# Kernel tuning notes

Hardware: AMD Instinct MI355X
Metric: run time of the kernel (lower is better)

## Reference

```python
import jax, jax.numpy as jnp
import numpy as np

DECAY = 0.99
EPS = 1e-05


def setup_inputs() -> dict:
    key = jax.random.key(0)
    k1, k2 = jax.random.split(key)
    x = jax.random.normal(k1, (32, 2048, 128), dtype=jnp.float32)
    embed = jax.random.normal(k2, (1024, 128), dtype=jnp.float32)
    cluster_size = jnp.zeros((1024,), dtype=jnp.float32)
    embed_avg = embed  # register_buffer('embed_avg', embed.clone())
    return {"x": x, "embed": embed, "cluster_size": cluster_size, "embed_avg": embed_avg}


def reference(x, embed, cluster_size, embed_avg):
    N, D = embed.shape
    flat_x = x.reshape(-1, D)  # [T, D]
    distances = (
        jnp.sum(flat_x * flat_x, axis=1, keepdims=True)
        + jnp.sum(embed * embed, axis=1)
        - 2.0 * flat_x @ embed.T
    )  # [T, N]
    idx = jnp.argmin(distances, axis=1)  # [T]
    quantized = embed[idx].reshape(x.shape)
    # EMA codebook update (training branch); segment_sum replaces the one-hot matmuls
    counts = jax.ops.segment_sum(jnp.ones(flat_x.shape[0], dtype=x.dtype), idx, num_segments=N)
    embed_sums = jax.ops.segment_sum(flat_x, idx, num_segments=N)  # [N, D]
    new_cluster_size = DECAY * cluster_size + (1.0 - DECAY) * counts
    new_embed_avg = DECAY * embed_avg + (1.0 - DECAY) * embed_sums
    n = jnp.sum(new_cluster_size)
    cs = (new_cluster_size + EPS) / (n + N * EPS) * n
    new_embed = new_embed_avg / cs[:, None]
    # straight-through estimator
    out = x + jax.lax.stop_gradient(quantized - x)
    return out, new_embed, new_cluster_size, new_embed_avg
```

## Files before the change

### kernel.cpp

```cpp
#include <hip/hip_runtime.h>

#define NTOK   65536
#define NCODES 1024
#define DIM    128
#define BT     128
#define MARGIN 6.0f
#define CAP    2047

typedef __attribute__((ext_vector_type(8))) short short8;
typedef __attribute__((ext_vector_type(4))) float f32x4;
typedef const __attribute__((address_space(1))) char gchar_t;
typedef __attribute__((address_space(3))) char lchar_t;

__device__ __forceinline__ unsigned short f2bf(float f) {
  unsigned u = __float_as_uint(f);
  u += 0x7FFFu + ((u >> 16) & 1u);
  return (unsigned short)(u >> 16);
}

__global__ __launch_bounds__(256) void ee_kernel(const float* __restrict__ E,
                                                 float* __restrict__ ee) {
  #pragma clang fp contract(off)
  int c = blockIdx.x * blockDim.x + threadIdx.x;
  if (c >= NCODES) return;
  const float4* r4 = (const float4*)(E + (size_t)c * DIM);
  float v[DIM];
  #pragma unroll
  for (int i = 0; i < 32; ++i) {
    float4 q = r4[i];
    v[4*i] = q.x; v[4*i+1] = q.y; v[4*i+2] = q.z; v[4*i+3] = q.w;
  }
  float r[8];
  #pragma unroll
  for (int j = 0; j < 8; ++j) r[j] = v[j] * v[j];
  #pragma unroll
  for (int i = 1; i < 16; ++i) {
    #pragma unroll
    for (int j = 0; j < 8; ++j) { float s = v[8*i+j] * v[8*i+j]; r[j] = r[j] + s; }
  }
  ee[c] = ((r[0]+r[1])+(r[2]+r[3])) + ((r[4]+r[5])+(r[6]+r[7]));
}

__global__ __launch_bounds__(256) void ebf_kernel(const float* __restrict__ E,
                                                  unsigned short* __restrict__ ebf) {
  const int id = blockIdx.x * 256 + threadIdx.x;
  const int l  = id & 63;
  const int s  = (id >> 6) & 3;
  const int ct = id >> 8;
  const int c  = ct * 16 + (l & 15);
  const int ko = s * 32 + (l >> 4) * 8;
  const float4* p = (const float4*)(E + (size_t)c * DIM + ko);
  float4 A = p[0], B = p[1];
  short8 v;
  v[0]=f2bf(A.x); v[1]=f2bf(A.y); v[2]=f2bf(A.z); v[3]=f2bf(A.w);
  v[4]=f2bf(B.x); v[5]=f2bf(B.y); v[6]=f2bf(B.z); v[7]=f2bf(B.w);
  ((short8*)ebf)[id] = v;
}

__global__ __launch_bounds__(256, 2) void vq_main(
    const float* __restrict__ X, const float* __restrict__ E,
    const unsigned short* __restrict__ ebf, const float* __restrict__ ee,
    float* __restrict__ out, int* __restrict__ idxg, int* __restrict__ cnt_i) {
  #pragma clang fp contract(off)
  __shared__ __align__(16) char e_lds[2 * 32768];
  __shared__ __align__(16) char region[10240];

  const int tid  = threadIdx.x;
  const int lane = tid & 63;
  const int wv   = tid >> 6;
  const long blk = blockIdx.x;
  const float* Xb = X + (size_t)blk * BT * DIM;

  float* thrf = (float*)region;
  unsigned long long* best64 = (unsigned long long*)(region + 512);
  int*      cand_n = (int*)(region + 1536);
  unsigned* cand   = (unsigned*)(region + 1540);

#define STAGE_E(CT, BUF)                                                      \
  {                                                                           \
    _Pragma("unroll")                                                         \
    for (int q = 0; q < 8; ++q) {                                             \
      const int u = wv * 8 + q;                                               \
      gchar_t* src = (gchar_t*)((const char*)ebf                              \
                      + ((size_t)(((CT) * 32 + u) * 64 + lane) << 4));        \
      lchar_t* dst = (lchar_t*)(e_lds + (BUF) * 32768 + u * 1024);            \
      __builtin_amdgcn_global_load_lds(                                       \
          (const __attribute__((address_space(1))) void*)src,                 \
          (__attribute__((address_space(3))) void*)dst, 16, 0, 0);            \
    }                                                                         \
  }

  STAGE_E(0, 0)

  short8 afr[2][4];
  #pragma unroll
  for (int t2 = 0; t2 < 2; ++t2) {
    const int row = (wv * 2 + t2) * 16 + (lane & 15);
    #pragma unroll
    for (int s = 0; s < 4; ++s) {
      const float4* p = (const float4*)(Xb + row * DIM + (s * 4 + (lane >> 4)) * 8);
      float4 A = p[0], B = p[1];
      short8 v;
      v[0]=f2bf(A.x); v[1]=f2bf(A.y); v[2]=f2bf(A.z); v[3]=f2bf(A.w);
      v[4]=f2bf(B.x); v[5]=f2bf(B.y); v[6]=f2bf(B.z); v[7]=f2bf(B.w);
      afr[t2][s] = v;
    }
  }

  float bv[2][4];
  #pragma unroll
  for (int t2 = 0; t2 < 2; ++t2)
    #pragma unroll
    for (int rg = 0; rg < 4; ++rg) bv[t2][rg] = __builtin_inff();

  asm volatile("s_waitcnt vmcnt(0)" ::: "memory");
  __syncthreads();

  for (int ctile = 0; ctile < 8; ++ctile) {
    if (ctile < 7) STAGE_E(ctile + 1, (ctile + 1) & 1)
    const char* eb = e_lds + (ctile & 1) * 32768;
    #pragma unroll 2
    for (int ct = 0; ct < 8; ++ct) {
      short8 b0 = *(const short8*)(eb + (ct * 4 + 0) * 1024 + lane * 16);
      short8 b1 = *(const short8*)(eb + (ct * 4 + 1) * 1024 + lane * 16);
      short8 b2 = *(const short8*)(eb + (ct * 4 + 2) * 1024 + lane * 16);
      short8 b3 = *(const short8*)(eb + (ct * 4 + 3) * 1024 + lane * 16);
      float eevv = ee[ctile * 128 + ct * 16 + (lane & 15)];
      #pragma unroll
      for (int t2 = 0; t2 < 2; ++t2) {
        f32x4 acc = {0.f, 0.f, 0.f, 0.f};
        acc = __builtin_amdgcn_mfma_f32_16x16x32_bf16(afr[t2][0], b0, acc, 0, 0, 0);
        acc = __builtin_amdgcn_mfma_f32_16x16x32_bf16(afr[t2][1], b1, acc, 0, 0, 0);
        acc = __builtin_amdgcn_mfma_f32_16x16x32_bf16(afr[t2][2], b2, acc, 0, 0, 0);
        acc = __builtin_amdgcn_mfma_f32_16x16x32_bf16(afr[t2][3], b3, acc, 0, 0, 0);
        #pragma unroll
        for (int rg = 0; rg < 4; ++rg) {
          float d = eevv - 2.0f * acc[rg];
          if (d < bv[t2][rg]) bv[t2][rg] = d;
        }
      }
    }
    asm volatile("s_waitcnt vmcnt(0)" ::: "memory");
    __syncthreads();
  }

  #pragma unroll
  for (int t2 = 0; t2 < 2; ++t2)
    #pragma unroll
    for (int rg = 0; rg < 4; ++rg) {
      float b = bv[t2][rg];
      #pragma unroll
      for (int m = 1; m < 16; m <<= 1) {
        float pb = __shfl_xor(b, m, 64);
        if (pb < b) b = pb;
      }
      if ((lane & 15) == 0)
        thrf[(wv * 2 + t2) * 16 + (lane >> 4) * 4 + rg] = b + MARGIN;
    }
  __syncthreads();
  if (tid < 128) best64[tid] = ~0ull;
  if (tid == 0) *cand_n = 0;
  __syncthreads();

  float thv[2][4];
  #pragma unroll
  for (int t2 = 0; t2 < 2; ++t2)
    #pragma unroll
    for (int rg = 0; rg < 4; ++rg)
      thv[t2][rg] = thrf[(wv * 2 + t2) * 16 + (lane >> 4) * 4 + rg];

  STAGE_E(0, 0)
  asm volatile("s_waitcnt vmcnt(0)" ::: "memory");
  __syncthreads();
  for (int ctile = 0; ctile < 8; ++ctile) {
    if (ctile < 7) STAGE_E(ctile + 1, (ctile + 1) & 1)
    const char* eb = e_lds + (ctile & 1) * 32768;
    #pragma unroll 2
    for (int ct = 0; ct < 8; ++ct) {
      short8 b0 = *(const short8*)(eb + (ct * 4 + 0) * 1024 + lane * 16);
      short8 b1 = *(const short8*)(eb + (ct * 4 + 1) * 1024 + lane * 16);
      short8 b2 = *(const short8*)(eb + (ct * 4 + 2) * 1024 + lane * 16);
      short8 b3 = *(const short8*)(eb + (ct * 4 + 3) * 1024 + lane * 16);
      float eevv = ee[ctile * 128 + ct * 16 + (lane & 15)];
      const int code = ctile * 128 + ct * 16 + (lane & 15);
      #pragma unroll
      for (int t2 = 0; t2 < 2; ++t2) {
        f32x4 acc = {0.f, 0.f, 0.f, 0.f};
        acc = __builtin_amdgcn_mfma_f32_16x16x32_bf16(afr[t2][0], b0, acc, 0, 0, 0);
        acc = __builtin_amdgcn_mfma_f32_16x16x32_bf16(afr[t2][1], b1, acc, 0, 0, 0);
        acc = __builtin_amdgcn_mfma_f32_16x16x32_bf16(afr[t2][2], b2, acc, 0, 0, 0);
        acc = __builtin_amdgcn_mfma_f32_16x16x32_bf16(afr[t2][3], b3, acc, 0, 0, 0);
        #pragma unroll
        for (int rg = 0; rg < 4; ++rg) {
          float d = eevv - 2.0f * acc[rg];
          if (d < thv[t2][rg]) {
            int slot = atomicAdd(cand_n, 1);
            if (slot < CAP) {
              const int token = (wv * 2 + t2) * 16 + (lane >> 4) * 4 + rg;
              cand[slot] = ((unsigned)token << 10) | (unsigned)code;
            }
          }
        }
      }
    }
    asm volatile("s_waitcnt vmcnt(0)" ::: "memory");
    __syncthreads();
  }
  __syncthreads();

  {
    int cn = *cand_n;
    const int nc = cn < CAP ? cn : CAP;
    for (int i = tid; i < nc; i += 256) {
      const unsigned pc = cand[i];
      const int t = pc >> 10, c = pc & 1023;
      const float* xr = Xb + t * DIM;
      const float* er = E + (size_t)c * DIM;
      float dot = 0.0f;
      #pragma unroll
      for (int k = 0; k < DIM; ++k) dot = __builtin_fmaf(xr[k], er[k], dot);
      float d = ee[c] - 2.0f * dot;
      unsigned u = __float_as_uint(d);
      u ^= (unsigned)((int)u >> 31) | 0x80000000u;
      unsigned long long key = ((unsigned long long)u << 32) | (unsigned)c;
      atomicMin(best64 + t, key);
    }
  }
  __syncthreads();

  if (tid < BT) {
    const int c0 = (int)(best64[tid] & 1023ull);
    idxg[blk * BT + tid] = c0;
    atomicAdd(cnt_i + c0, 1);
  }
  const int tt2 = tid >> 1, hf = tid & 1;
  const int fi2 = (int)(best64[tt2] & 1023ull);
  const float* xrow = Xb  + tt2 * DIM + hf * 64;
  const float* erow = E   + ((size_t)fi2 << 7) + hf * 64;
  float*       orow = out + ((size_t)blk * BT + tt2) * DIM + hf * 64;
  #pragma unroll
  for (int q = 0; q < 16; ++q) {
    float4 xv = *(const float4*)(xrow + q * 4);
    float4 ev = *(const float4*)(erow + q * 4);
    float4 o;
    o.x = xv.x + (ev.x - xv.x);
    o.y = xv.y + (ev.y - xv.y);
    o.z = xv.z + (ev.z - xv.z);
    o.w = xv.w + (ev.w - xv.w);
    *(float4*)(orow + q * 4) = o;
  }
}

__global__ __launch_bounds__(1024) void prefix_fin1(
    const float* __restrict__ cluster_size, const int* __restrict__ cnt_i,
    float* __restrict__ out_cs, float* __restrict__ cs_ws,
    int* __restrict__ cursor, int* __restrict__ offs) {
  #pragma clang fp contract(off)
  __shared__ float red[1024];
  __shared__ int   sc[1024];
  const int n = threadIdx.x;
  const int cnt = cnt_i[n];
  float ncs = 0.99f * cluster_size[n] + 0.01f * (float)cnt;
  out_cs[n] = ncs;
  red[n] = ncs;
  sc[n]  = cnt;
  __syncthreads();
  for (int s = 512; s > 0; s >>= 1) {
    if (n < s) red[n] = red[n] + red[n + s];
    __syncthreads();
  }
  float ntot = red[0];
  cs_ws[n] = (ncs + 1e-5f) / (ntot + 0.01024f) * ntot;
  for (int d = 1; d < 1024; d <<= 1) {
    int t = (n >= d) ? sc[n - d] : 0;
    __syncthreads();
    sc[n] += t;
    __syncthreads();
  }
  int excl = sc[n] - cnt;
  cursor[n] = excl;
  offs[n]   = excl;
}

__global__ __launch_bounds__(256) void scatter_kernel(
    const int* __restrict__ idxg, int* __restrict__ cursor,
    int* __restrict__ order) {
  const int t  = blockIdx.x * 256 + threadIdx.x;
  const int fi = idxg[t];
  const int slot = atomicAdd(cursor + fi, 1);
  order[slot] = t;
}

__global__ __launch_bounds__(256) void sums_chunk(
    const float* __restrict__ X, const int* __restrict__ order,
    const int* __restrict__ idxg, float* __restrict__ sums) {
  #pragma clang fp contract(off)
  const int lane = threadIdx.x & 63;
  const int base = blockIdx.x * 256 + (threadIdx.x >> 6) * 64;
  const int tl = order[base + lane];
  const int cl = idxg[tl];
  float ax = 0.f, ay = 0.f;
  int cprev = __shfl(cl, 0, 64);
  #pragma unroll
  for (int j0 = 0; j0 < 64; j0 += 8) {
    int tj[8], cj[8];
    float2 buf[8];
    #pragma unroll
    for (int q = 0; q < 8; ++q) tj[q] = __shfl(tl, j0 + q, 64);
    #pragma unroll
    for (int q = 0; q < 8; ++q)
      buf[q] = *((const float2*)(X + ((size_t)tj[q] << 7)) + lane);
    #pragma unroll
    for (int q = 0; q < 8; ++q) cj[q] = __shfl(cl, j0 + q, 64);
    #pragma unroll
    for (int q = 0; q < 8; ++q) {
      if (cj[q] != cprev) {
        atomicAdd(sums + cprev * DIM + lane * 2,     ax);
        atomicAdd(sums + cprev * DIM + lane * 2 + 1, ay);
        ax = 0.f; ay = 0.f; cprev = cj[q];
      }
      ax = ax + buf[q].x;
      ay = ay + buf[q].y;
    }
  }
  atomicAdd(sums + cprev * DIM + lane * 2,     ax);
  atomicAdd(sums + cprev * DIM + lane * 2 + 1, ay);
}

__global__ __launch_bounds__(256) void finalize2(
    const float* __restrict__ embed_avg, const float* __restrict__ sums,
    const float* __restrict__ cs_ws, float* __restrict__ out_embed,
    float* __restrict__ out_avg) {
  #pragma clang fp contract(off)
  int i = blockIdx.x * 256 + threadIdx.x;
  float av = 0.99f * embed_avg[i] + 0.01f * sums[i];
  out_avg[i]   = av;
  out_embed[i] = av / cs_ws[i >> 7];
}

extern "C" void kernel_launch(void* const* d_in, const int* in_sizes, int n_in,
                              void* d_out, int out_size, void* d_ws, size_t ws_size,
                              hipStream_t stream) {
  const float* X  = (const float*)d_in[0];
  const float* E  = (const float*)d_in[1];
  const float* CS = (const float*)d_in[2];
  const float* EA = (const float*)d_in[3];
  float* out = (float*)d_out;
  float* ws  = (float*)d_ws;

  int*   cnt_i  = (int*)ws;
  float* sums   = ws + 1024;
  float* eearr  = ws + 132096;
  float* csarr  = ws + 133120;
  int*   cursor = (int*)(ws + 134144);
  int*   offs   = (int*)(ws + 135168);
  int*   idxarr = (int*)(ws + 136192);
  int*   order  = (int*)(ws + 201728);
  unsigned short* ebf = (unsigned short*)(ws + 267264);

  hipMemsetAsync(d_ws, 0, 132096 * sizeof(float), stream);

  ee_kernel     <<<NCODES / 256, 256, 0, stream>>>(E, eearr);
  ebf_kernel    <<<64,           256, 0, stream>>>(E, ebf);
  vq_main       <<<NTOK / BT,    256, 0, stream>>>(X, E, ebf, eearr, out,
                                                   idxarr, cnt_i);
  prefix_fin1   <<<1, 1024, 0, stream>>>(CS, cnt_i, out + 8519680, csarr,
                                         cursor, offs);
  scatter_kernel<<<NTOK / 256,   256, 0, stream>>>(idxarr, cursor, order);
  sums_chunk    <<<NTOK / 256,   256, 0, stream>>>(X, order, idxarr, sums);
  finalize2     <<<131072 / 256, 256, 0, stream>>>(EA, sums, csarr,
                                                   out + 8388608, out + 8520704);
}
```

Measured before the change: 173.0 us.

## Keep codebook slices in registers and stream X tiles from LDS; merge prep kernels

Reverses the main loop's data reuse. Each wave now holds a 512-code slice of the bf16 codebook in registers, and the block's 128 tokens are staged once in LDS in MFMA fragment layout. This replaces the double-buffered global-to-LDS codebook staging and its per-tile barriers. Per-wave partial minima go to shared memory and are combined into the per-token thresholds. The two codebook preprocessing kernels are merged into one launch. The cost is a large register footprint (32 short8 fragments per wave), which may hurt occupancy under launch_bounds(256,2) or cause spills.

```diff
diff --git a/kernel.cpp b/kernel.cpp
--- a/kernel.cpp
+++ b/kernel.cpp
@@ -9,8 +9,6 @@
 
 typedef __attribute__((ext_vector_type(8))) short short8;
 typedef __attribute__((ext_vector_type(4))) float f32x4;
-typedef const __attribute__((address_space(1))) char gchar_t;
-typedef __attribute__((address_space(3))) char lchar_t;
 
 __device__ __forceinline__ unsigned short f2bf(float f) {
   unsigned u = __float_as_uint(f);
@@ -18,43 +16,43 @@
   return (unsigned short)(u >> 16);
 }
 
-__global__ __launch_bounds__(256) void ee_kernel(const float* __restrict__ E,
-                                                 float* __restrict__ ee) {
-  #pragma clang fp contract(off)
-  int c = blockIdx.x * blockDim.x + threadIdx.x;
-  if (c >= NCODES) return;
-  const float4* r4 = (const float4*)(E + (size_t)c * DIM);
-  float v[DIM];
-  #pragma unroll
-  for (int i = 0; i < 32; ++i) {
-    float4 q = r4[i];
-    v[4*i] = q.x; v[4*i+1] = q.y; v[4*i+2] = q.z; v[4*i+3] = q.w;
-  }
-  float r[8];
-  #pragma unroll
-  for (int j = 0; j < 8; ++j) r[j] = v[j] * v[j];
-  #pragma unroll
-  for (int i = 1; i < 16; ++i) {
-    #pragma unroll
-    for (int j = 0; j < 8; ++j) { float s = v[8*i+j] * v[8*i+j]; r[j] = r[j] + s; }
-  }
-  ee[c] = ((r[0]+r[1])+(r[2]+r[3])) + ((r[4]+r[5])+(r[6]+r[7]));
-}
-
-__global__ __launch_bounds__(256) void ebf_kernel(const float* __restrict__ E,
-                                                  unsigned short* __restrict__ ebf) {
-  const int id = blockIdx.x * 256 + threadIdx.x;
-  const int l  = id & 63;
-  const int s  = (id >> 6) & 3;
-  const int ct = id >> 8;
-  const int c  = ct * 16 + (l & 15);
-  const int ko = s * 32 + (l >> 4) * 8;
-  const float4* p = (const float4*)(E + (size_t)c * DIM + ko);
-  float4 A = p[0], B = p[1];
-  short8 v;
-  v[0]=f2bf(A.x); v[1]=f2bf(A.y); v[2]=f2bf(A.z); v[3]=f2bf(A.w);
-  v[4]=f2bf(B.x); v[5]=f2bf(B.y); v[6]=f2bf(B.z); v[7]=f2bf(B.w);
-  ((short8*)ebf)[id] = v;
+__global__ __launch_bounds__(256) void prep_kernel(const float* __restrict__ E,
+                                                   float* __restrict__ ee,
+                                                   unsigned short* __restrict__ ebf) {
+  #pragma clang fp contract(off)
+  const int b = blockIdx.x;
+  if (b < 64) {
+    const int id = b * 256 + threadIdx.x;
+    const int l  = id & 63;
+    const int s  = (id >> 6) & 3;
+    const int ct = id >> 8;
+    const int c  = ct * 16 + (l & 15);
+    const int ko = s * 32 + (l >> 4) * 8;
+    const float4* p = (const float4*)(E + (size_t)c * DIM + ko);
+    float4 A = p[0], B = p[1];
+    short8 v;
+    v[0]=f2bf(A.x); v[1]=f2bf(A.y); v[2]=f2bf(A.z); v[3]=f2bf(A.w);
+    v[4]=f2bf(B.x); v[5]=f2bf(B.y); v[6]=f2bf(B.z); v[7]=f2bf(B.w);
+    ((short8*)ebf)[id] = v;
+  } else {
+    const int c = (b - 64) * 256 + threadIdx.x;
+    const float4* r4 = (const float4*)(E + (size_t)c * DIM);
+    float v[DIM];
+    #pragma unroll
+    for (int i = 0; i < 32; ++i) {
+      float4 q = r4[i];
+      v[4*i] = q.x; v[4*i+1] = q.y; v[4*i+2] = q.z; v[4*i+3] = q.w;
+    }
+    float r[8];
+    #pragma unroll
+    for (int j = 0; j < 8; ++j) r[j] = v[j] * v[j];
+    #pragma unroll
+    for (int i = 1; i < 16; ++i) {
+      #pragma unroll
+      for (int j = 0; j < 8; ++j) { float s = v[8*i+j] * v[8*i+j]; r[j] = r[j] + s; }
+    }
+    ee[c] = ((r[0]+r[1])+(r[2]+r[3])) + ((r[4]+r[5])+(r[6]+r[7]));
+  }
 }
 
 __global__ __launch_bounds__(256, 2) void vq_main(
@@ -62,8 +60,12 @@
     const unsigned short* __restrict__ ebf, const float* __restrict__ ee,
     float* __restrict__ out, int* __restrict__ idxg, int* __restrict__ cnt_i) {
   #pragma clang fp contract(off)
-  __shared__ __align__(16) char e_lds[2 * 32768];
-  __shared__ __align__(16) char region[10240];
+  __shared__ __align__(16) char x_lds[32768];
+  __shared__ float bestA[4][BT];
+  __shared__ float thrf[BT];
+  __shared__ unsigned long long best64[BT];
+  __shared__ int cand_n;
+  __shared__ unsigned cand[CAP];
 
   const int tid  = threadIdx.x;
   const int lane = tid & 63;
@@ -71,145 +73,133 @@
   const long blk = blockIdx.x;
   const float* Xb = X + (size_t)blk * BT * DIM;
 
-  float* thrf = (float*)region;
-  unsigned long long* best64 = (unsigned long long*)(region + 512);
-  int*      cand_n = (int*)(region + 1536);
-  unsigned* cand   = (unsigned*)(region + 1540);
-
-#define STAGE_E(CT, BUF)                                                      \
-  {                                                                           \
-    _Pragma("unroll")                                                         \
-    for (int q = 0; q < 8; ++q) {                                             \
-      const int u = wv * 8 + q;                                               \
-      gchar_t* src = (gchar_t*)((const char*)ebf                              \
-                      + ((size_t)(((CT) * 32 + u) * 64 + lane) << 4));        \
-      lchar_t* dst = (lchar_t*)(e_lds + (BUF) * 32768 + u * 1024);            \
-      __builtin_amdgcn_global_load_lds(                                       \
-          (const __attribute__((address_space(1))) void*)src,                 \
-          (__attribute__((address_space(3))) void*)dst, 16, 0, 0);            \
-    }                                                                         \
-  }
-
-  STAGE_E(0, 0)
-
-  short8 afr[2][4];
-  #pragma unroll
-  for (int t2 = 0; t2 < 2; ++t2) {
-    const int row = (wv * 2 + t2) * 16 + (lane & 15);
-    #pragma unroll
-    for (int s = 0; s < 4; ++s) {
-      const float4* p = (const float4*)(Xb + row * DIM + (s * 4 + (lane >> 4)) * 8);
-      float4 A = p[0], B = p[1];
+  {
+    const int r = tid >> 1, h = tid & 1;
+    const float4* p4 = (const float4*)(Xb + r * DIM + h * 64);
+    #pragma unroll
+    for (int q = 0; q < 8; ++q) {
+      float4 A = p4[2*q], B = p4[2*q+1];
       short8 v;
       v[0]=f2bf(A.x); v[1]=f2bf(A.y); v[2]=f2bf(A.z); v[3]=f2bf(A.w);
       v[4]=f2bf(B.x); v[5]=f2bf(B.y); v[6]=f2bf(B.z); v[7]=f2bf(B.w);
-      afr[t2][s] = v;
-    }
-  }
-
-  float bv[2][4];
-  #pragma unroll
-  for (int t2 = 0; t2 < 2; ++t2)
-    #pragma unroll
-    for (int rg = 0; rg < 4; ++rg) bv[t2][rg] = __builtin_inff();
-
-  asm volatile("s_waitcnt vmcnt(0)" ::: "memory");
-  __syncthreads();
-
-  for (int ctile = 0; ctile < 8; ++ctile) {
-    if (ctile < 7) STAGE_E(ctile + 1, (ctile + 1) & 1)
-    const char* eb = e_lds + (ctile & 1) * 32768;
-    #pragma unroll 2
-    for (int ct = 0; ct < 8; ++ct) {
-      short8 b0 = *(const short8*)(eb + (ct * 4 + 0) * 1024 + lane * 16);
-      short8 b1 = *(const short8*)(eb + (ct * 4 + 1) * 1024 + lane * 16);
-      short8 b2 = *(const short8*)(eb + (ct * 4 + 2) * 1024 + lane * 16);
-      short8 b3 = *(const short8*)(eb + (ct * 4 + 3) * 1024 + lane * 16);
-      float eevv = ee[ctile * 128 + ct * 16 + (lane & 15)];
-      #pragma unroll
-      for (int t2 = 0; t2 < 2; ++t2) {
-        f32x4 acc = {0.f, 0.f, 0.f, 0.f};
-        acc = __builtin_amdgcn_mfma_f32_16x16x32_bf16(afr[t2][0], b0, acc, 0, 0, 0);
-        acc = __builtin_amdgcn_mfma_f32_16x16x32_bf16(afr[t2][1], b1, acc, 0, 0, 0);
-        acc = __builtin_amdgcn_mfma_f32_16x16x32_bf16(afr[t2][2], b2, acc, 0, 0, 0);
-        acc = __builtin_amdgcn_mfma_f32_16x16x32_bf16(afr[t2][3], b3, acc, 0, 0, 0);
-        #pragma unroll
-        for (int rg = 0; rg < 4; ++rg) {
-          float d = eevv - 2.0f * acc[rg];
-          if (d < bv[t2][rg]) bv[t2][rg] = d;
-        }
-      }
-    }
-    asm volatile("s_waitcnt vmcnt(0)" ::: "memory");
-    __syncthreads();
-  }
-
-  #pragma unroll
-  for (int t2 = 0; t2 < 2; ++t2)
-    #pragma unroll
-    for (int rg = 0; rg < 4; ++rg) {
-      float b = bv[t2][rg];
-      #pragma unroll
-      for (int m = 1; m < 16; m <<= 1) {
-        float pb = __shfl_xor(b, m, 64);
-        if (pb < b) b = pb;
-      }
-      if ((lane & 15) == 0)
-        thrf[(wv * 2 + t2) * 16 + (lane >> 4) * 4 + rg] = b + MARGIN;
-    }
-  __syncthreads();
-  if (tid < 128) best64[tid] = ~0ull;
-  if (tid == 0) *cand_n = 0;
-  __syncthreads();
-
-  float thv[2][4];
-  #pragma unroll
-  for (int t2 = 0; t2 < 2; ++t2)
-    #pragma unroll
-    for (int rg = 0; rg < 4; ++rg)
-      thv[t2][rg] = thrf[(wv * 2 + t2) * 16 + (lane >> 4) * 4 + rg];
-
-  STAGE_E(0, 0)
-  asm volatile("s_waitcnt vmcnt(0)" ::: "memory");
-  __syncthreads();
-  for (int ctile = 0; ctile < 8; ++ctile) {
-    if (ctile < 7) STAGE_E(ctile + 1, (ctile + 1) & 1)
-    const char* eb = e_lds + (ctile & 1) * 32768;
-    #pragma unroll 2
-    for (int ct = 0; ct < 8; ++ct) {
-      short8 b0 = *(const short8*)(eb + (ct * 4 + 0) * 1024 + lane * 16);
-      short8 b1 = *(const short8*)(eb + (ct * 4 + 1) * 1024 + lane * 16);
-      short8 b2 = *(const short8*)(eb + (ct * 4 + 2) * 1024 + lane * 16);
-      short8 b3 = *(const short8*)(eb + (ct * 4 + 3) * 1024 + lane * 16);
-      float eevv = ee[ctile * 128 + ct * 16 + (lane & 15)];
-      const int code = ctile * 128 + ct * 16 + (lane & 15);
-      #pragma unroll
-      for (int t2 = 0; t2 < 2; ++t2) {
-        f32x4 acc = {0.f, 0.f, 0.f, 0.f};
-        acc = __builtin_amdgcn_mfma_f32_16x16x32_bf16(afr[t2][0], b0, acc, 0, 0, 0);
-        acc = __builtin_amdgcn_mfma_f32_16x16x32_bf16(afr[t2][1], b1, acc, 0, 0, 0);
-        acc = __builtin_amdgcn_mfma_f32_16x16x32_bf16(afr[t2][2], b2, acc, 0, 0, 0);
-        acc = __builtin_amdgcn_mfma_f32_16x16x32_bf16(afr[t2][3], b3, acc, 0, 0, 0);
-        #pragma unroll
-        for (int rg = 0; rg < 4; ++rg) {
-          float d = eevv - 2.0f * acc[rg];
-          if (d < thv[t2][rg]) {
-            int slot = atomicAdd(cand_n, 1);
-            if (slot < CAP) {
-              const int token = (wv * 2 + t2) * 16 + (lane >> 4) * 4 + rg;
-              cand[slot] = ((unsigned)token << 10) | (unsigned)code;
-            }
-          }
-        }
-      }
-    }
-    asm volatile("s_waitcnt vmcnt(0)" ::: "memory");
-    __syncthreads();
-  }
+      const int o    = h * 8 + q;
+      const int unit = (r >> 4) * 4 + (o >> 2);
+      const int ln   = ((o & 3) << 4) | (r & 15);
+      *(short8*)(x_lds + unit * 1024 + ln * 16) = v;
+    }
+  }
+
+  short8 bfr[8][4];
+  float  eev[8];
+  const short8* ebv = (const short8*)ebf;
+
+#define LOAD_SET(SET)                                                         \
+  { _Pragma("unroll")                                                         \
+    for (int ct = 0; ct < 8; ++ct) {                                          \
+      _Pragma("unroll")                                                       \
+      for (int s = 0; s < 4; ++s)                                             \
+        bfr[ct][s] = ebv[(((SET) * 32 + wv * 8 + ct) * 4 + s) * 64 + lane];   \
+      eev[ct] = ee[(SET) * 512 + wv * 128 + ct * 16 + (lane & 15)];           \
+    } }
+
+#define MFMA4(ACC, A0, A1, A2, A3, CT)                                        \
+  ACC = __builtin_amdgcn_mfma_f32_16x16x32_bf16(A0, bfr[CT][0], ACC, 0, 0, 0);\
+  ACC = __builtin_amdgcn_mfma_f32_16x16x32_bf16(A1, bfr[CT][1], ACC, 0, 0, 0);\
+  ACC = __builtin_amdgcn_mfma_f32_16x16x32_bf16(A2, bfr[CT][2], ACC, 0, 0, 0);\
+  ACC = __builtin_amdgcn_mfma_f32_16x16x32_bf16(A3, bfr[CT][3], ACC, 0, 0, 0);
+
+#define SWEEP_MIN(FIRST)                                                      \
+  for (int tt = 0; tt < 8; ++tt) {                                            \
+    const char* xb = x_lds + tt * 4096 + lane * 16;                           \
+    short8 a0 = *(const short8*)(xb);                                         \
+    short8 a1 = *(const short8*)(xb + 1024);                                  \
+    short8 a2 = *(const short8*)(xb + 2048);                                  \
+    short8 a3 = *(const short8*)(xb + 3072);                                  \
+    float bv0 = __builtin_inff(), bv1 = __builtin_inff();                     \
+    float bv2 = __builtin_inff(), bv3 = __builtin_inff();                     \
+    _Pragma("unroll")                                                         \
+    for (int ct = 0; ct < 8; ++ct) {                                          \
+      f32x4 acc = {0.f, 0.f, 0.f, 0.f};                                       \
+      MFMA4(acc, a0, a1, a2, a3, ct)                                          \
+      float d0 = eev[ct] - 2.0f * acc[0]; if (d0 < bv0) bv0 = d0;             \
+      float d1 = eev[ct] - 2.0f * acc[1]; if (d1 < bv1) bv1 = d1;             \
+      float d2 = eev[ct] - 2.0f * acc[2]; if (d2 < bv2) bv2 = d2;             \
+      float d3 = eev[ct] - 2.0f * acc[3]; if (d3 < bv3) bv3 = d3;             \
+    }                                                                         \
+    _Pragma("unroll")                                                         \
+    for (int m = 1; m < 16; m <<= 1) {                                        \
+      float p0 = __shfl_xor(bv0, m, 64); if (p0 < bv0) bv0 = p0;              \
+      float p1 = __shfl_xor(bv1, m, 64); if (p1 < bv1) bv1 = p1;              \
+      float p2 = __shfl_xor(bv2, m, 64); if (p2 < bv2) bv2 = p2;              \
+      float p3 = __shfl_xor(bv3, m, 64); if (p3 < bv3) bv3 = p3;              \
+    }                                                                         \
+    if ((lane & 15) == 0) {                                                   \
+      const int tok = tt * 16 + (lane >> 4) * 4;                              \
+      if (FIRST) {                                                            \
+        bestA[wv][tok]     = bv0; bestA[wv][tok + 1] = bv1;                   \
+        bestA[wv][tok + 2] = bv2; bestA[wv][tok + 3] = bv3;                   \
+      } else {                                                                \
+        if (bv0 < bestA[wv][tok])     bestA[wv][tok]     = bv0;               \
+        if (bv1 < bestA[wv][tok + 1]) bestA[wv][tok + 1] = bv1;               \
+        if (bv2 < bestA[wv][tok + 2]) bestA[wv][tok + 2] = bv2;               \
+        if (bv3 < bestA[wv][tok + 3]) bestA[wv][tok + 3] = bv3;               \
+      }                                                                       \
+    }                                                                         \
+  }
+
+#define EMIT(D, RG, TH, CODE, TT)                                             \
+  if ((D) < (TH)) {                                                           \
+    int sl = atomicAdd(&cand_n, 1);                                           \
+    if (sl < CAP)                                                             \
+      cand[sl] = ((unsigned)((TT) * 16 + (lane >> 4) * 4 + (RG)) << 10)       \
+               | (unsigned)(CODE);                                            \
+  }
+
+#define SWEEP_EMIT(CB)                                                        \
+  for (int tt = 0; tt < 8; ++tt) {                                            \
+    const char* xb = x_lds + tt * 4096 + lane * 16;                           \
+    short8 a0 = *(const short8*)(xb);                                         \
+    short8 a1 = *(const short8*)(xb + 1024);                                  \
+    short8 a2 = *(const short8*)(xb + 2048);                                  \
+    short8 a3 = *(const short8*)(xb + 3072);                                  \
+    const float4 th4 = *(const float4*)(thrf + tt * 16 + (lane >> 4) * 4);    \
+    _Pragma("unroll")                                                         \
+    for (int ct = 0; ct < 8; ++ct) {                                          \
+      f32x4 acc = {0.f, 0.f, 0.f, 0.f};                                       \
+      MFMA4(acc, a0, a1, a2, a3, ct)                                          \
+      const int code = (CB) + ct * 16 + (lane & 15);                          \
+      float d0 = eev[ct] - 2.0f * acc[0]; EMIT(d0, 0, th4.x, code, tt)        \
+      float d1 = eev[ct] - 2.0f * acc[1]; EMIT(d1, 1, th4.y, code, tt)        \
+      float d2 = eev[ct] - 2.0f * acc[2]; EMIT(d2, 2, th4.z, code, tt)        \
+      float d3 = eev[ct] - 2.0f * acc[3]; EMIT(d3, 3, th4.w, code, tt)        \
+    }                                                                         \
+  }
+
+  LOAD_SET(0)
+  __syncthreads();
+
+  SWEEP_MIN(1)
+  LOAD_SET(1)
+  SWEEP_MIN(0)
+  __syncthreads();
+
+  if (tid < BT) {
+    float m0 = bestA[0][tid], m1 = bestA[1][tid];
+    float m2 = bestA[2][tid], m3 = bestA[3][tid];
+    float mm = fminf(fminf(m0, m1), fminf(m2, m3));
+    thrf[tid]   = mm + MARGIN;
+    best64[tid] = ~0ull;
+  }
+  if (tid == 0) cand_n = 0;
+  __syncthreads();
+
+  SWEEP_EMIT(512 + wv * 128)
+  LOAD_SET(0)
+  SWEEP_EMIT(wv * 128)
   __syncthreads();
 
   {
-    int cn = *cand_n;
+    int cn = cand_n;
     const int nc = cn < CAP ? cn : CAP;
     for (int i = tid; i < nc; i += 256) {
       const unsigned pc = cand[i];
@@ -360,8 +350,7 @@
 
   hipMemsetAsync(d_ws, 0, 132096 * sizeof(float), stream);
 
-  ee_kernel     <<<NCODES / 256, 256, 0, stream>>>(E, eearr);
-  ebf_kernel    <<<64,           256, 0, stream>>>(E, ebf);
+  prep_kernel   <<<68,           256, 0, stream>>>(E, eearr, ebf);
   vq_main       <<<NTOK / BT,    256, 0, stream>>>(X, E, ebf, eearr, out,
                                                    idxarr, cnt_i);
   prefix_fin1   <<<1, 1024, 0, stream>>>(CS, cnt_i, out + 8519680, csarr,
```

New measurement: 165.0 us. -4.6%, faster.

## Split codebook across waves with per-wave LDS staging and fuse prep kernels

Applied to the files above, without the earlier changes.

The token tile per block shrinks to 64. Each of the four waves now scans a private quarter of the codebook for all 64 tokens, double-buffered in its own LDS slice, so the per-tile block-wide barriers go away. Per-wave minima are merged through shared memory to form the rescoring threshold. The ee computation, bf16 codebook conversion and workspace zeroing are fused into one prep launch, ee is cached in LDS as bf16, occupancy is raised to four blocks per CU, and blocks are swizzled. The candidate cap drops and the coarse ee loses precision, which relies on the margin plus the exact fp32 rescore.

```diff
diff --git a/kernel.cpp b/kernel.cpp
--- a/kernel.cpp
+++ b/kernel.cpp
@@ -3,9 +3,9 @@
 #define NTOK   65536
 #define NCODES 1024
 #define DIM    128
-#define BT     128
+#define BT     64
 #define MARGIN 6.0f
-#define CAP    2047
+#define CAP    960
 
 typedef __attribute__((ext_vector_type(8))) short short8;
 typedef __attribute__((ext_vector_type(4))) float f32x4;
@@ -18,84 +18,81 @@
   return (unsigned short)(u >> 16);
 }
 
-__global__ __launch_bounds__(256) void ee_kernel(const float* __restrict__ E,
-                                                 float* __restrict__ ee) {
-  #pragma clang fp contract(off)
-  int c = blockIdx.x * blockDim.x + threadIdx.x;
-  if (c >= NCODES) return;
-  const float4* r4 = (const float4*)(E + (size_t)c * DIM);
-  float v[DIM];
-  #pragma unroll
-  for (int i = 0; i < 32; ++i) {
-    float4 q = r4[i];
-    v[4*i] = q.x; v[4*i+1] = q.y; v[4*i+2] = q.z; v[4*i+3] = q.w;
-  }
-  float r[8];
-  #pragma unroll
-  for (int j = 0; j < 8; ++j) r[j] = v[j] * v[j];
-  #pragma unroll
-  for (int i = 1; i < 16; ++i) {
-    #pragma unroll
-    for (int j = 0; j < 8; ++j) { float s = v[8*i+j] * v[8*i+j]; r[j] = r[j] + s; }
-  }
-  ee[c] = ((r[0]+r[1])+(r[2]+r[3])) + ((r[4]+r[5])+(r[6]+r[7]));
-}
-
-__global__ __launch_bounds__(256) void ebf_kernel(const float* __restrict__ E,
-                                                  unsigned short* __restrict__ ebf) {
-  const int id = blockIdx.x * 256 + threadIdx.x;
-  const int l  = id & 63;
-  const int s  = (id >> 6) & 3;
-  const int ct = id >> 8;
-  const int c  = ct * 16 + (l & 15);
-  const int ko = s * 32 + (l >> 4) * 8;
-  const float4* p = (const float4*)(E + (size_t)c * DIM + ko);
-  float4 A = p[0], B = p[1];
-  short8 v;
-  v[0]=f2bf(A.x); v[1]=f2bf(A.y); v[2]=f2bf(A.z); v[3]=f2bf(A.w);
-  v[4]=f2bf(B.x); v[5]=f2bf(B.y); v[6]=f2bf(B.z); v[7]=f2bf(B.w);
-  ((short8*)ebf)[id] = v;
-}
-
-__global__ __launch_bounds__(256, 2) void vq_main(
+__global__ __launch_bounds__(256) void prep_kernel(const float* __restrict__ E,
+                                                   float* __restrict__ ee,
+                                                   unsigned short* __restrict__ ebf,
+                                                   float* __restrict__ zero_base) {
+  #pragma clang fp contract(off)
+  const int b = blockIdx.x;
+  if (b < 64) {
+    const int id = b * 256 + threadIdx.x;
+    const int l  = id & 63;
+    const int s  = (id >> 6) & 3;
+    const int ct = id >> 8;
+    const int c  = ct * 16 + (l & 15);
+    const int ko = s * 32 + (l >> 4) * 8;
+    const float4* p = (const float4*)(E + (size_t)c * DIM + ko);
+    float4 A = p[0], B = p[1];
+    short8 v;
+    v[0]=f2bf(A.x); v[1]=f2bf(A.y); v[2]=f2bf(A.z); v[3]=f2bf(A.w);
+    v[4]=f2bf(B.x); v[5]=f2bf(B.y); v[6]=f2bf(B.z); v[7]=f2bf(B.w);
+    ((short8*)ebf)[id] = v;
+  } else if (b < 68) {
+    const int c = (b - 64) * 256 + threadIdx.x;
+    const float4* r4 = (const float4*)(E + (size_t)c * DIM);
+    float v[DIM];
+    #pragma unroll
+    for (int i = 0; i < 32; ++i) {
+      float4 q = r4[i];
+      v[4*i] = q.x; v[4*i+1] = q.y; v[4*i+2] = q.z; v[4*i+3] = q.w;
+    }
+    float r[8];
+    #pragma unroll
+    for (int j = 0; j < 8; ++j) r[j] = v[j] * v[j];
+    #pragma unroll
+    for (int i = 1; i < 16; ++i) {
+      #pragma unroll
+      for (int j = 0; j < 8; ++j) { float s = v[8*i+j] * v[8*i+j]; r[j] = r[j] + s; }
+    }
+    ee[c] = ((r[0]+r[1])+(r[2]+r[3])) + ((r[4]+r[5])+(r[6]+r[7]));
+  } else {
+    float4 z = {0.f, 0.f, 0.f, 0.f};
+    ((float4*)zero_base)[(b - 68) * 256 + threadIdx.x] = z;
+  }
+}
+
+__global__ __launch_bounds__(256, 4) void vq_main(
     const float* __restrict__ X, const float* __restrict__ E,
     const unsigned short* __restrict__ ebf, const float* __restrict__ ee,
     float* __restrict__ out, int* __restrict__ idxg, int* __restrict__ cnt_i) {
   #pragma clang fp contract(off)
-  __shared__ __align__(16) char e_lds[2 * 32768];
-  __shared__ __align__(16) char region[10240];
+  __shared__ __align__(16) char e_lds[4 * 8192];
+  __shared__ __align__(16) unsigned short eebf[NCODES];
+  __shared__ __align__(16) float bestA[4][BT];
+  __shared__ __align__(16) float thrf[BT];
+  __shared__ __align__(16) unsigned long long best64[BT];
+  __shared__ int cand_n;
+  __shared__ unsigned cand[CAP];
 
   const int tid  = threadIdx.x;
   const int lane = tid & 63;
   const int wv   = tid >> 6;
-  const long blk = blockIdx.x;
+  const int bid  = blockIdx.x;
+  const long blk = (bid & 7) * 128 + (bid >> 3);
   const float* Xb = X + (size_t)blk * BT * DIM;
 
-  float* thrf = (float*)region;
-  unsigned long long* best64 = (unsigned long long*)(region + 512);
-  int*      cand_n = (int*)(region + 1536);
-  unsigned* cand   = (unsigned*)(region + 1540);
-
-#define STAGE_E(CT, BUF)                                                      \
-  {                                                                           \
-    _Pragma("unroll")                                                         \
-    for (int q = 0; q < 8; ++q) {                                             \
-      const int u = wv * 8 + q;                                               \
-      gchar_t* src = (gchar_t*)((const char*)ebf                              \
-                      + ((size_t)(((CT) * 32 + u) * 64 + lane) << 4));        \
-      lchar_t* dst = (lchar_t*)(e_lds + (BUF) * 32768 + u * 1024);            \
-      __builtin_amdgcn_global_load_lds(                                       \
-          (const __attribute__((address_space(1))) void*)src,                 \
-          (__attribute__((address_space(3))) void*)dst, 16, 0, 0);            \
-    }                                                                         \
-  }
-
-  STAGE_E(0, 0)
-
-  short8 afr[2][4];
-  #pragma unroll
-  for (int t2 = 0; t2 < 2; ++t2) {
-    const int row = (wv * 2 + t2) * 16 + (lane & 15);
+  {
+    float4 e4 = *((const float4*)ee + tid);
+    eebf[tid * 4 + 0] = f2bf(e4.x);
+    eebf[tid * 4 + 1] = f2bf(e4.y);
+    eebf[tid * 4 + 2] = f2bf(e4.z);
+    eebf[tid * 4 + 3] = f2bf(e4.w);
+  }
+
+  short8 afr[4][4];
+  #pragma unroll
+  for (int tt = 0; tt < 4; ++tt) {
+    const int row = tt * 16 + (lane & 15);
     #pragma unroll
     for (int s = 0; s < 4; ++s) {
       const float4* p = (const float4*)(Xb + row * DIM + (s * 4 + (lane >> 4)) * 8);
@@ -103,113 +100,121 @@
       short8 v;
       v[0]=f2bf(A.x); v[1]=f2bf(A.y); v[2]=f2bf(A.z); v[3]=f2bf(A.w);
       v[4]=f2bf(B.x); v[5]=f2bf(B.y); v[6]=f2bf(B.z); v[7]=f2bf(B.w);
-      afr[t2][s] = v;
-    }
-  }
-
-  float bv[2][4];
-  #pragma unroll
-  for (int t2 = 0; t2 < 2; ++t2)
-    #pragma unroll
-    for (int rg = 0; rg < 4; ++rg) bv[t2][rg] = __builtin_inff();
-
-  asm volatile("s_waitcnt vmcnt(0)" ::: "memory");
-  __syncthreads();
-
-  for (int ctile = 0; ctile < 8; ++ctile) {
-    if (ctile < 7) STAGE_E(ctile + 1, (ctile + 1) & 1)
-    const char* eb = e_lds + (ctile & 1) * 32768;
-    #pragma unroll 2
-    for (int ct = 0; ct < 8; ++ct) {
-      short8 b0 = *(const short8*)(eb + (ct * 4 + 0) * 1024 + lane * 16);
-      short8 b1 = *(const short8*)(eb + (ct * 4 + 1) * 1024 + lane * 16);
-      short8 b2 = *(const short8*)(eb + (ct * 4 + 2) * 1024 + lane * 16);
-      short8 b3 = *(const short8*)(eb + (ct * 4 + 3) * 1024 + lane * 16);
-      float eevv = ee[ctile * 128 + ct * 16 + (lane & 15)];
-      #pragma unroll
-      for (int t2 = 0; t2 < 2; ++t2) {
-        f32x4 acc = {0.f, 0.f, 0.f, 0.f};
-        acc = __builtin_amdgcn_mfma_f32_16x16x32_bf16(afr[t2][0], b0, acc, 0, 0, 0);
-        acc = __builtin_amdgcn_mfma_f32_16x16x32_bf16(afr[t2][1], b1, acc, 0, 0, 0);
-        acc = __builtin_amdgcn_mfma_f32_16x16x32_bf16(afr[t2][2], b2, acc, 0, 0, 0);
-        acc = __builtin_amdgcn_mfma_f32_16x16x32_bf16(afr[t2][3], b3, acc, 0, 0, 0);
-        #pragma unroll
-        for (int rg = 0; rg < 4; ++rg) {
-          float d = eevv - 2.0f * acc[rg];
-          if (d < bv[t2][rg]) bv[t2][rg] = d;
-        }
+      afr[tt][s] = v;
+    }
+  }
+
+  char* myl = e_lds + wv * 8192;
+#define STAGE(CT, BUF)                                                        \
+  { _Pragma("unroll")                                                         \
+    for (int s = 0; s < 4; ++s) {                                             \
+      gchar_t* src = (gchar_t*)((const char*)ebf                              \
+          + ((size_t)((((wv * 16 + (CT)) * 4 + s) * 64) + lane) << 4));       \
+      lchar_t* dst = (lchar_t*)(myl + (BUF) * 4096 + s * 1024);               \
+      __builtin_amdgcn_global_load_lds(                                       \
+          (const __attribute__((address_space(1))) void*)src,                 \
+          (__attribute__((address_space(3))) void*)dst, 16, 0, 0);            \
+    } }
+
+#define MFMA4(ACC, TT)                                                        \
+  ACC = __builtin_amdgcn_mfma_f32_16x16x32_bf16(afr[TT][0], b0, ACC, 0, 0, 0);\
+  ACC = __builtin_amdgcn_mfma_f32_16x16x32_bf16(afr[TT][1], b1, ACC, 0, 0, 0);\
+  ACC = __builtin_amdgcn_mfma_f32_16x16x32_bf16(afr[TT][2], b2, ACC, 0, 0, 0);\
+  ACC = __builtin_amdgcn_mfma_f32_16x16x32_bf16(afr[TT][3], b3, ACC, 0, 0, 0);
+
+  STAGE(0, 0)
+  __syncthreads();
+
+  float bv[4][4];
+  #pragma unroll
+  for (int tt = 0; tt < 4; ++tt)
+    #pragma unroll
+    for (int rg = 0; rg < 4; ++rg) bv[tt][rg] = __builtin_inff();
+
+  for (int ct = 0; ct < 16; ++ct) {
+    STAGE((ct + 1) & 15, (ct + 1) & 1)
+    asm volatile("s_waitcnt vmcnt(4)" ::: "memory");
+    const char* eb = myl + (ct & 1) * 4096;
+    short8 b0 = *(const short8*)(eb +    0 + lane * 16);
+    short8 b1 = *(const short8*)(eb + 1024 + lane * 16);
+    short8 b2 = *(const short8*)(eb + 2048 + lane * 16);
+    short8 b3 = *(const short8*)(eb + 3072 + lane * 16);
+    const unsigned short eu = eebf[(wv * 16 + ct) * 16 + (lane & 15)];
+    const float ev = __uint_as_float((unsigned)eu << 16);
+    #pragma unroll
+    for (int tt = 0; tt < 4; ++tt) {
+      f32x4 acc = {0.f, 0.f, 0.f, 0.f};
+      MFMA4(acc, tt)
+      #pragma unroll
+      for (int rg = 0; rg < 4; ++rg) {
+        float d = ev - 2.0f * acc[rg];
+        if (d < bv[tt][rg]) bv[tt][rg] = d;
       }
     }
-    asm volatile("s_waitcnt vmcnt(0)" ::: "memory");
-    __syncthreads();
-  }
-
-  #pragma unroll
-  for (int t2 = 0; t2 < 2; ++t2)
+  }
+
+  #pragma unroll
+  for (int tt = 0; tt < 4; ++tt)
     #pragma unroll
     for (int rg = 0; rg < 4; ++rg) {
-      float b = bv[t2][rg];
+      float b = bv[tt][rg];
       #pragma unroll
       for (int m = 1; m < 16; m <<= 1) {
         float pb = __shfl_xor(b, m, 64);
         if (pb < b) b = pb;
       }
       if ((lane & 15) == 0)
-        thrf[(wv * 2 + t2) * 16 + (lane >> 4) * 4 + rg] = b + MARGIN;
-    }
-  __syncthreads();
-  if (tid < 128) best64[tid] = ~0ull;
-  if (tid == 0) *cand_n = 0;
-  __syncthreads();
-
-  float thv[2][4];
-  #pragma unroll
-  for (int t2 = 0; t2 < 2; ++t2)
+        bestA[wv][tt * 16 + (lane >> 4) * 4 + rg] = b;
+    }
+  __syncthreads();
+
+  if (tid < BT) {
+    float m0 = bestA[0][tid], m1 = bestA[1][tid];
+    float m2 = bestA[2][tid], m3 = bestA[3][tid];
+    thrf[tid]   = fminf(fminf(m0, m1), fminf(m2, m3)) + MARGIN;
+    best64[tid] = ~0ull;
+  }
+  if (tid == 0) cand_n = 0;
+  __syncthreads();
+
+  float thv[4][4];
+  #pragma unroll
+  for (int tt = 0; tt < 4; ++tt)
     #pragma unroll
     for (int rg = 0; rg < 4; ++rg)
-      thv[t2][rg] = thrf[(wv * 2 + t2) * 16 + (lane >> 4) * 4 + rg];
-
-  STAGE_E(0, 0)
-  asm volatile("s_waitcnt vmcnt(0)" ::: "memory");
-  __syncthreads();
-  for (int ctile = 0; ctile < 8; ++ctile) {
-    if (ctile < 7) STAGE_E(ctile + 1, (ctile + 1) & 1)
-    const char* eb = e_lds + (ctile & 1) * 32768;
-    #pragma unroll 2
-    for (int ct = 0; ct < 8; ++ct) {
-      short8 b0 = *(const short8*)(eb + (ct * 4 + 0) * 1024 + lane * 16);
-      short8 b1 = *(const short8*)(eb + (ct * 4 + 1) * 1024 + lane * 16);
-      short8 b2 = *(const short8*)(eb + (ct * 4 + 2) * 1024 + lane * 16);
-      short8 b3 = *(const short8*)(eb + (ct * 4 + 3) * 1024 + lane * 16);
-      float eevv = ee[ctile * 128 + ct * 16 + (lane & 15)];
-      const int code = ctile * 128 + ct * 16 + (lane & 15);
-      #pragma unroll
-      for (int t2 = 0; t2 < 2; ++t2) {
-        f32x4 acc = {0.f, 0.f, 0.f, 0.f};
-        acc = __builtin_amdgcn_mfma_f32_16x16x32_bf16(afr[t2][0], b0, acc, 0, 0, 0);
-        acc = __builtin_amdgcn_mfma_f32_16x16x32_bf16(afr[t2][1], b1, acc, 0, 0, 0);
-        acc = __builtin_amdgcn_mfma_f32_16x16x32_bf16(afr[t2][2], b2, acc, 0, 0, 0);
-        acc = __builtin_amdgcn_mfma_f32_16x16x32_bf16(afr[t2][3], b3, acc, 0, 0, 0);
-        #pragma unroll
-        for (int rg = 0; rg < 4; ++rg) {
-          float d = eevv - 2.0f * acc[rg];
-          if (d < thv[t2][rg]) {
-            int slot = atomicAdd(cand_n, 1);
-            if (slot < CAP) {
-              const int token = (wv * 2 + t2) * 16 + (lane >> 4) * 4 + rg;
-              cand[slot] = ((unsigned)token << 10) | (unsigned)code;
-            }
-          }
+      thv[tt][rg] = thrf[tt * 16 + (lane >> 4) * 4 + rg];
+
+  for (int ct = 0; ct < 16; ++ct) {
+    STAGE((ct + 1) & 15, (ct + 1) & 1)
+    asm volatile("s_waitcnt vmcnt(4)" ::: "memory");
+    const char* eb = myl + (ct & 1) * 4096;
+    short8 b0 = *(const short8*)(eb +    0 + lane * 16);
+    short8 b1 = *(const short8*)(eb + 1024 + lane * 16);
+    short8 b2 = *(const short8*)(eb + 2048 + lane * 16);
+    short8 b3 = *(const short8*)(eb + 3072 + lane * 16);
+    const int code = (wv * 16 + ct) * 16 + (lane & 15);
+    const unsigned short eu = eebf[code];
+    const float ev = __uint_as_float((unsigned)eu << 16);
+    #pragma unroll
+    for (int tt = 0; tt < 4; ++tt) {
+      f32x4 acc = {0.f, 0.f, 0.f, 0.f};
+      MFMA4(acc, tt)
+      #pragma unroll
+      for (int rg = 0; rg < 4; ++rg) {
+        float d = ev - 2.0f * acc[rg];
+        if (d < thv[tt][rg]) {
+          int sl = atomicAdd(&cand_n, 1);
+          if (sl < CAP)
+            cand[sl] = ((unsigned)(tt * 16 + (lane >> 4) * 4 + rg) << 10)
+                     | (unsigned)code;
         }
       }
     }
-    asm volatile("s_waitcnt vmcnt(0)" ::: "memory");
-    __syncthreads();
   }
   __syncthreads();
 
   {
-    int cn = *cand_n;
+    int cn = cand_n;
     const int nc = cn < CAP ? cn : CAP;
     for (int i = tid; i < nc; i += 256) {
       const unsigned pc = cand[i];
@@ -233,13 +238,13 @@
     idxg[blk * BT + tid] = c0;
     atomicAdd(cnt_i + c0, 1);
   }
-  const int tt2 = tid >> 1, hf = tid & 1;
+  const int tt2 = tid >> 2, hf = tid & 3;
   const int fi2 = (int)(best64[tt2] & 1023ull);
-  const float* xrow = Xb  + tt2 * DIM + hf * 64;
-  const float* erow = E   + ((size_t)fi2 << 7) + hf * 64;
-  float*       orow = out + ((size_t)blk * BT + tt2) * DIM + hf * 64;
-  #pragma unroll
-  for (int q = 0; q < 16; ++q) {
+  const float* xrow = Xb  + tt2 * DIM + hf * 32;
+  const float* erow = E   + ((size_t)fi2 << 7) + hf * 32;
+  float*       orow = out + ((size_t)blk * BT + tt2) * DIM + hf * 32;
+  #pragma unroll
+  for (int q = 0; q < 8; ++q) {
     float4 xv = *(const float4*)(xrow + q * 4);
     float4 ev = *(const float4*)(erow + q * 4);
     float4 o;
@@ -358,10 +363,7 @@
   int*   order  = (int*)(ws + 201728);
   unsigned short* ebf = (unsigned short*)(ws + 267264);
 
-  hipMemsetAsync(d_ws, 0, 132096 * sizeof(float), stream);
-
-  ee_kernel     <<<NCODES / 256, 256, 0, stream>>>(E, eearr);
-  ebf_kernel    <<<64,           256, 0, stream>>>(E, ebf);
+  prep_kernel   <<<197,          256, 0, stream>>>(E, eearr, ebf, ws);
   vq_main       <<<NTOK / BT,    256, 0, stream>>>(X, E, ebf, eearr, out,
                                                    idxarr, cnt_i);
   prefix_fin1   <<<1, 1024, 0, stream>>>(CS, cnt_i, out + 8519680, csarr,
```

After: 159.5 us (median of 2 runs). 7.8% less time.
